# Kernel tuning notes

Measured on AMD Instinct MI355X. Metric: run time of the kernel, lower is better.

The kernel has to match this reference:

```python
import jax, jax.numpy as jnp
import numpy as np
import math

B, S, D, H = 2, 2048, 1024, 16
HD = D // H
EPS = 1e-05


def gelu(x):
    # tanh-approx GELU as in the torch source
    return 0.5 * x * (1.0 + jnp.tanh(jnp.sqrt(2.0 / jnp.pi) * (x + 0.044715 * x ** 3)))


def layernorm(x, w, b):
    # NOTE: torch .std() uses Bessel correction (ddof=1) and eps is added to std
    u = jnp.mean(x, axis=-1, keepdims=True)
    xc = x - u
    s = jnp.sqrt(jnp.sum(xc * xc, axis=-1, keepdims=True) / (x.shape[-1] - 1))
    return w * (xc / (s + EPS)) + b


def setup_inputs() -> dict:
    key = jax.random.key(0)
    ks = jax.random.split(key, 8)
    std = 0.02
    # weights stored [in, out] (transposed vs torch Linear) so y = x @ W + b
    return {
        "x": jax.random.normal(ks[0], (B, S, D), jnp.float32),
        "ln1_w": jnp.ones((D,), jnp.float32),
        "ln1_b": jnp.zeros((D,), jnp.float32),
        "c_attn_w": jax.random.normal(ks[1], (D, 3 * D), jnp.float32) * std,
        "c_attn_b": jnp.zeros((3 * D,), jnp.float32),
        "c_proj_w": jax.random.normal(ks[2], (D, D), jnp.float32) * std,
        "c_proj_b": jnp.zeros((D,), jnp.float32),
        "ln2_w": jnp.ones((D,), jnp.float32),
        "ln2_b": jnp.zeros((D,), jnp.float32),
        "fc_w": jax.random.normal(ks[3], (D, 4 * D), jnp.float32) * std,
        "fc_b": jnp.zeros((4 * D,), jnp.float32),
        "proj_w": jax.random.normal(ks[4], (4 * D, D), jnp.float32) * std,
        "proj_b": jnp.zeros((D,), jnp.float32),
    }


def attention(x, c_attn_w, c_attn_b, c_proj_w, c_proj_b):
    qkv = x @ c_attn_w + c_attn_b                      # [B,S,3D]
    q, k, v = jnp.split(qkv, 3, axis=-1)
    q = q.reshape(B, S, H, HD)
    k = k.reshape(B, S, H, HD)
    v = v.reshape(B, S, H, HD)
    w = jnp.einsum("bqhd,bkhd->bhqk", q, k) / math.sqrt(HD)  # scale=True
    bias = jnp.tril(jnp.ones((S, S), jnp.float32))     # causal mask
    w = w * bias - 1e10 * (1.0 - bias)
    w = jax.nn.softmax(w, axis=-1)
    a = jnp.einsum("bhqk,bkhd->bqhd", w, v).reshape(B, S, D)
    return a @ c_proj_w + c_proj_b


def reference(x, ln1_w, ln1_b, c_attn_w, c_attn_b, c_proj_w, c_proj_b,
              ln2_w, ln2_b, fc_w, fc_b, proj_w, proj_b):
    a = attention(layernorm(x, ln1_w, ln1_b), c_attn_w, c_attn_b, c_proj_w, c_proj_b)
    x = x + a
    h = gelu(layernorm(x, ln2_w, ln2_b) @ fc_w + fc_b)
    m = h @ proj_w + proj_b
    return x + m
```

## Files before the change

### kernel.cpp

```cpp
#include <hip/hip_runtime.h>

typedef unsigned short u16;
typedef __attribute__((ext_vector_type(8))) short short8;
typedef __attribute__((ext_vector_type(4))) float floatx4;

__device__ __forceinline__ float bf2f(u16 u) {
  unsigned int v = ((unsigned int)u) << 16;
  return __builtin_bit_cast(float, v);
}
__device__ __forceinline__ u16 f2bf(float f) {
  unsigned int u = __builtin_bit_cast(unsigned int, f);
  u += 0x7FFFu + ((u >> 16) & 1u);
  return (u16)(u >> 16);
}
__device__ __forceinline__ void gload_lds16(const void* g, void* l) {
  __builtin_amdgcn_global_load_lds(
      (const __attribute__((address_space(1))) unsigned int*)g,
      (__attribute__((address_space(3))) unsigned int*)l, 16, 0, 0);
}

__global__ __launch_bounds__(256) void transpose_f32_bf16(const float* __restrict__ in,
                                                          u16* __restrict__ out,
                                                          int K, int N) {
  __shared__ float tile[32][33];
  int n0 = blockIdx.x * 32, k0 = blockIdx.y * 32;
  int tx = threadIdx.x & 31, ty = threadIdx.x >> 5;
#pragma unroll
  for (int i = 0; i < 4; i++) {
    int r = ty + i * 8;
    tile[r][tx] = in[(size_t)(k0 + r) * N + n0 + tx];
  }
  __syncthreads();
#pragma unroll
  for (int i = 0; i < 4; i++) {
    int r = ty + i * 8;
    out[(size_t)(n0 + r) * K + k0 + tx] = f2bf(tile[tx][r]);
  }
}

__global__ __launch_bounds__(256) void ln_f32(const float* __restrict__ xin,
                                              const float* __restrict__ wgt,
                                              const float* __restrict__ bia,
                                              u16* __restrict__ out) {
  int row = blockIdx.x, t = threadIdx.x;
  const float* xr = xin + (size_t)row * 1024 + t * 4;
  float4 f = *(const float4*)xr;
  float v[4] = {f.x, f.y, f.z, f.w};
  float s1 = v[0] + v[1] + v[2] + v[3];
  float s2 = v[0] * v[0] + v[1] * v[1] + v[2] * v[2] + v[3] * v[3];
#pragma unroll
  for (int off = 32; off; off >>= 1) {
    s1 += __shfl_down(s1, off);
    s2 += __shfl_down(s2, off);
  }
  __shared__ float red[8];
  int lane = t & 63, w = t >> 6;
  if (lane == 0) { red[w] = s1; red[4 + w] = s2; }
  __syncthreads();
  s1 = red[0] + red[1] + red[2] + red[3];
  s2 = red[4] + red[5] + red[6] + red[7];
  float mean = s1 * (1.f / 1024.f);
  float var = (s2 - 1024.f * mean * mean) * (1.f / 1023.f);
  var = var < 0.f ? 0.f : var;
  float inv = 1.f / (sqrtf(var) + 1e-5f);
  float4 wv = *(const float4*)(wgt + t * 4);
  float4 bv = *(const float4*)(bia + t * 4);
  float wa[4] = {wv.x, wv.y, wv.z, wv.w};
  float ba[4] = {bv.x, bv.y, bv.z, bv.w};
#pragma unroll
  for (int j = 0; j < 4; j++)
    out[(size_t)row * 1024 + t * 4 + j] = f2bf(wa[j] * ((v[j] - mean) * inv) + ba[j]);
}

template <int EPI>
__global__ __launch_bounds__(256) void gemm_bt(const u16* __restrict__ A,
                                               const u16* __restrict__ Bt,
                                               const float* __restrict__ bias,
                                               const float* __restrict__ res,
                                               void* __restrict__ outp,
                                               void* __restrict__ outp2,
                                               int msplit,
                                               int ldc, int K) {
  __shared__ __align__(16) u16 As[2][128 * 64];
  __shared__ __align__(16) u16 Bs[2][128 * 64];
  int tid = threadIdx.x;
  int lane = tid & 63, w = tid >> 6;
  int quad = lane >> 4, c16 = lane & 15;
  int wm = w >> 1, wn = w & 1;
  int nbx = gridDim.x;
  int nwg = nbx * gridDim.y;
  int bid = blockIdx.y * nbx + blockIdx.x;
  int swz = (bid & 7) * (nwg >> 3) + (bid >> 3);
  int bn = swz % nbx, bm = swz / nbx;
  const u16* Ab = A + (size_t)bm * 128 * K;
  const u16* Bb = Bt + (size_t)bn * 128 * K;

  int rbase = tid >> 3;
  int csrc = (((tid & 7) ^ ((tid >> 3) & 7))) * 8;
  int dbase = w * 512;

  floatx4 zf = {0.f, 0.f, 0.f, 0.f};
  floatx4 acc[4][4];
#pragma unroll
  for (int i = 0; i < 4; i++)
#pragma unroll
    for (int j = 0; j < 4; j++) acc[i][j] = zf;

  auto stage = [&](int kt, int sl) {
    const u16* At = Ab + kt * 64;
    const u16* Bt2 = Bb + kt * 64;
#pragma unroll
    for (int j = 0; j < 4; j++) {
      int r = j * 32 + rbase;
      gload_lds16(At + (size_t)r * K + csrc, &As[sl][j * 2048 + dbase]);
      gload_lds16(Bt2 + (size_t)r * K + csrc, &Bs[sl][j * 2048 + dbase]);
    }
  };

  int nt = K >> 6;
  stage(0, 0);
  int sl = 0;
  for (int t = 0; t < nt; ++t) {
    if (t + 1 < nt) {
      stage(t + 1, sl ^ 1);
      asm volatile("s_waitcnt vmcnt(8)" ::: "memory");
    } else {
      asm volatile("s_waitcnt vmcnt(0)" ::: "memory");
    }
    __builtin_amdgcn_s_barrier();
    __builtin_amdgcn_sched_barrier(0);
    const u16* as = As[sl];
    const u16* bs = Bs[sl];
#pragma unroll
    for (int ks = 0; ks < 2; ++ks) {
      int col = (ks * 32 + quad * 8) ^ ((c16 & 7) * 8);
      short8 af[4], bfr[4];
#pragma unroll
      for (int mt = 0; mt < 4; mt++)
        af[mt] = *(const short8*)&as[(wm * 64 + mt * 16 + c16) * 64 + col];
#pragma unroll
      for (int nt2 = 0; nt2 < 4; nt2++)
        bfr[nt2] = *(const short8*)&bs[(wn * 64 + nt2 * 16 + c16) * 64 + col];
#pragma unroll
      for (int mt = 0; mt < 4; mt++)
#pragma unroll
        for (int nt2 = 0; nt2 < 4; nt2++)
          acc[mt][nt2] = __builtin_amdgcn_mfma_f32_16x16x32_bf16(af[mt], bfr[nt2], acc[mt][nt2], 0, 0, 0);
    }
    __builtin_amdgcn_s_barrier();
    __builtin_amdgcn_sched_barrier(0);
    sl ^= 1;
  }

  int gm0 = bm * 128 + wm * 64;
  int gn0 = bn * 128 + wn * 64;
#pragma unroll
  for (int nt2 = 0; nt2 < 4; nt2++) {
    int gn = gn0 + nt2 * 16 + c16;
    float bia = 0.f;
    if constexpr (EPI != 3) bia = bias[gn];
#pragma unroll
    for (int mt = 0; mt < 4; mt++) {
#pragma unroll
      for (int r = 0; r < 4; r++) {
        int gm = gm0 + mt * 16 + quad * 4 + r;
        float v = acc[mt][nt2][r] + bia;
        if constexpr (EPI == 0) {
          void* op = outp;
          int gmo = gm;
          if (gm >= msplit) { op = outp2; gmo = gm - msplit; }
          ((u16*)op)[(size_t)gmo * ldc + gn] = f2bf(v);
        } else if constexpr (EPI == 1) {
          size_t o = (size_t)gm * ldc + gn;
          ((float*)outp)[o] = v + res[o];
        } else if constexpr (EPI == 2) {
          size_t o = (size_t)gm * ldc + gn;
          float g = 0.5f * v * (1.f + tanhf(0.7978845608f * (v + 0.044715f * v * v * v)));
          ((u16*)outp)[o] = f2bf(g);
        } else {
          size_t o = (size_t)gm * ldc + gn;
          ((float*)outp)[o] += v;
        }
      }
    }
  }
}

__device__ __forceinline__ void attn_process(
    const short8& qf0, const short8& qf1,
    float* m_run, float* l_run, floatx4* oacc,
    const u16* __restrict__ Ks, const u16* __restrict__ Vt, u16* __restrict__ pw,
    int kt, int qt, int w, int quad, int c16, bool diag) {
  floatx4 zf = {0.f, 0.f, 0.f, 0.f};
  floatx4 s[4];
#pragma unroll
  for (int n = 0; n < 4; n++) {
    short8 kf0 = *(const short8*)&Ks[(n * 16 + c16) * 72 + quad * 8];
    short8 kf1 = *(const short8*)&Ks[(n * 16 + c16) * 72 + 32 + quad * 8];
    floatx4 a = zf;
    a = __builtin_amdgcn_mfma_f32_16x16x32_bf16(qf0, kf0, a, 0, 0, 0);
    a = __builtin_amdgcn_mfma_f32_16x16x32_bf16(qf1, kf1, a, 0, 0, 0);
    s[n] = a;
  }
  if (diag) {
#pragma unroll
    for (int n = 0; n < 4; n++) {
      int kg = kt * 64 + n * 16 + c16;
#pragma unroll
      for (int r = 0; r < 4; r++) {
        int qg = qt * 64 + w * 16 + quad * 4 + r;
        s[n][r] = (kg > qg) ? -1e30f : s[n][r];
      }
    }
  }
  float mt[4];
#pragma unroll
  for (int r = 0; r < 4; r++)
    mt[r] = fmaxf(fmaxf(s[0][r], s[1][r]), fmaxf(s[2][r], s[3][r]));
#pragma unroll
  for (int off = 1; off < 16; off <<= 1)
#pragma unroll
    for (int r = 0; r < 4; r++) mt[r] = fmaxf(mt[r], __shfl_xor(mt[r], off));
  float alpha[4], lsum[4];
#pragma unroll
  for (int r = 0; r < 4; r++) {
    float mn = fmaxf(m_run[r], mt[r]);
    alpha[r] = __expf(m_run[r] - mn);
    m_run[r] = mn;
    lsum[r] = 0.f;
  }
#pragma unroll
  for (int n = 0; n < 4; n++)
#pragma unroll
    for (int r = 0; r < 4; r++) {
      float p = __expf(s[n][r] - m_run[r]);
      s[n][r] = p;
      lsum[r] += p;
    }
#pragma unroll
  for (int off = 1; off < 16; off <<= 1)
#pragma unroll
    for (int r = 0; r < 4; r++) lsum[r] += __shfl_xor(lsum[r], off);
#pragma unroll
  for (int r = 0; r < 4; r++) l_run[r] = l_run[r] * alpha[r] + lsum[r];
#pragma unroll
  for (int c = 0; c < 4; c++)
#pragma unroll
    for (int r = 0; r < 4; r++) oacc[c][r] *= alpha[r];
#pragma unroll
  for (int n = 0; n < 4; n++)
#pragma unroll
    for (int r = 0; r < 4; r++)
      pw[(quad * 4 + r) * 72 + n * 16 + c16] = f2bf(s[n][r]);
  short8 pf0 = *(const short8*)&pw[c16 * 72 + quad * 8];
  short8 pf1 = *(const short8*)&pw[c16 * 72 + 32 + quad * 8];
#pragma unroll
  for (int c = 0; c < 4; c++) {
    int d = c * 16 + c16;
    short8 vf0 = *(const short8*)&Vt[d * 64 + ((quad * 8) ^ (d & 56))];
    short8 vf1 = *(const short8*)&Vt[d * 64 + ((32 + quad * 8) ^ (d & 56))];
    oacc[c] = __builtin_amdgcn_mfma_f32_16x16x32_bf16(pf0, vf0, oacc[c], 0, 0, 0);
    oacc[c] = __builtin_amdgcn_mfma_f32_16x16x32_bf16(pf1, vf1, oacc[c], 0, 0, 0);
  }
}

__device__ __forceinline__ short8 scale8_eighth(short8 v) {
  short8 r;
#pragma unroll
  for (int j = 0; j < 8; j++) {
    unsigned int b = ((unsigned int)(u16)v[j]) << 16;
    float f = __builtin_bit_cast(float, b) * 0.125f;
    r[j] = (short)(u16)(__builtin_bit_cast(unsigned int, f) >> 16);
  }
  return r;
}

__global__ __launch_bounds__(256) void attn_mfma2(const u16* __restrict__ qkv0,
                                                  const u16* __restrict__ qkv1,
                                                  u16* __restrict__ aout) {
  int pr = blockIdx.x, h = blockIdx.y;
  const u16* qkvb = blockIdx.z ? qkv1 : qkv0;
  aout += (size_t)blockIdx.z * 2048 * 1024;
  int qt0 = pr, qt1 = 31 - pr;
  int tid = threadIdx.x, lane = tid & 63, w = tid >> 6;
  int quad = lane >> 4, c16 = lane & 15;
  __shared__ __align__(16) u16 Ks[2][64 * 72];
  __shared__ __align__(16) u16 Vt[2][64 * 64];
  __shared__ __align__(16) u16 Ps[4][16 * 72];

  size_t qoffA = (size_t)(qt0 * 64 + w * 16 + c16) * 3072 + h * 64;
  short8 qfA0 = scale8_eighth(*(const short8*)(qkvb + qoffA + quad * 8));
  short8 qfA1 = scale8_eighth(*(const short8*)(qkvb + qoffA + 32 + quad * 8));
  size_t qoffB = (size_t)(qt1 * 64 + w * 16 + c16) * 3072 + h * 64;
  short8 qfB0 = scale8_eighth(*(const short8*)(qkvb + qoffB + quad * 8));
  short8 qfB1 = scale8_eighth(*(const short8*)(qkvb + qoffB + 32 + quad * 8));

  floatx4 zf = {0.f, 0.f, 0.f, 0.f};
  float mA[4], lA[4], mB[4], lB[4];
  floatx4 oA[4], oB[4];
#pragma unroll
  for (int r = 0; r < 4; r++) { mA[r] = -1e30f; lA[r] = 0.f; mB[r] = -1e30f; lB[r] = 0.f; }
#pragma unroll
  for (int c = 0; c < 4; c++) { oA[c] = zf; oB[c] = zf; }

  int srow = (tid * 2) >> 3;
  int sd8 = ((tid * 2) & 7) * 8;
  short8 kr0, kr1, vr0, vr1;

  auto issue = [&](int kt) {
    size_t gb = (size_t)(kt * 64 + srow) * 3072 + h * 64 + sd8;
    kr0 = *(const short8*)(qkvb + gb + 1024);
    kr1 = *(const short8*)(qkvb + gb + 1024 + 8);
    vr0 = *(const short8*)(qkvb + gb + 2048);
    vr1 = *(const short8*)(qkvb + gb + 2048 + 8);
  };
  auto commit = [&](int b) {
    *(short8*)&Ks[b][srow * 72 + sd8] = kr0;
    *(short8*)&Ks[b][srow * 72 + sd8 + 8] = kr1;
    u16* vt = Vt[b];
#pragma unroll
    for (int j = 0; j < 8; j++) {
      int d = sd8 + j;
      vt[d * 64 + (srow ^ (d & 56))] = (u16)vr0[j];
      int d2 = sd8 + 8 + j;
      vt[d2 * 64 + (srow ^ (d2 & 56))] = (u16)vr1[j];
    }
  };

  u16* pw = &Ps[w][0];
  int last = qt1;
  issue(0);
  commit(0);
  __syncthreads();
  int cur = 0;
  for (int kt = 0; kt <= last; ++kt) {
    if (kt < last) issue(kt + 1);

    attn_process(qfB0, qfB1, mB, lB, oB, Ks[cur], Vt[cur], pw, kt, qt1, w, quad, c16, kt == qt1);
    if (kt <= qt0)
      attn_process(qfA0, qfA1, mA, lA, oA, Ks[cur], Vt[cur], pw, kt, qt0, w, quad, c16, kt == qt0);

    if (kt < last) {
      commit(cur ^ 1);
      __syncthreads();
      cur ^= 1;
    }
  }

  size_t obA = (size_t)(qt0 * 64 + w * 16) * 1024 + h * 64;
  size_t obB = (size_t)(qt1 * 64 + w * 16) * 1024 + h * 64;
#pragma unroll
  for (int r = 0; r < 4; r++) {
    float invA = 1.f / lA[r], invB = 1.f / lB[r];
#pragma unroll
    for (int c = 0; c < 4; c++) {
      aout[obA + (size_t)(quad * 4 + r) * 1024 + c * 16 + c16] = f2bf(oA[c][r] * invA);
      aout[obB + (size_t)(quad * 4 + r) * 1024 + c * 16 + c16] = f2bf(oB[c][r] * invB);
    }
  }
}

extern "C" void kernel_launch(void* const* d_in, const int* in_sizes, int n_in,
                              void* d_out, int out_size, void* d_ws, size_t ws_size,
                              hipStream_t stream) {
  const float* x        = (const float*)d_in[0];
  const float* ln1_w    = (const float*)d_in[1];
  const float* ln1_b    = (const float*)d_in[2];
  const float* c_attn_w = (const float*)d_in[3];
  const float* c_attn_b = (const float*)d_in[4];
  const float* c_proj_w = (const float*)d_in[5];
  const float* c_proj_b = (const float*)d_in[6];
  const float* ln2_w    = (const float*)d_in[7];
  const float* ln2_b    = (const float*)d_in[8];
  const float* fc_w     = (const float*)d_in[9];
  const float* fc_b     = (const float*)d_in[10];
  const float* proj_w   = (const float*)d_in[11];
  const float* proj_b   = (const float*)d_in[12];

  char* ws = (char*)d_ws;
  const size_t MiB = 1u << 20;
  const int BIG = 1 << 30;

  u16* wt_attn  = (u16*)(ws + 0);
  u16* wt_cproj = (u16*)(ws + 6 * MiB);
  u16* ln1b     = (u16*)(ws + 8 * MiB);
  u16* qkv1     = (u16*)(ws + 16 * MiB);
  u16* qkv0     = (u16*)d_out;
  u16* attn_out = (u16*)(ws + 8 * MiB);
  float* x1     = (float*)d_out;

  transpose_f32_bf16<<<dim3(96, 32), 256, 0, stream>>>(c_attn_w, wt_attn, 1024, 3072);
  transpose_f32_bf16<<<dim3(32, 32), 256, 0, stream>>>(c_proj_w, wt_cproj, 1024, 1024);
  ln_f32<<<4096, 256, 0, stream>>>(x, ln1_w, ln1_b, ln1b);
  gemm_bt<0><<<dim3(24, 32), 256, 0, stream>>>(ln1b, wt_attn, c_attn_b, nullptr,
                                               qkv0, qkv1, 2048, 3072, 1024);
  attn_mfma2<<<dim3(16, 16, 2), 256, 0, stream>>>(qkv0, qkv1, attn_out);
  gemm_bt<1><<<dim3(8, 32), 256, 0, stream>>>(attn_out, wt_cproj, c_proj_b, x,
                                              x1, nullptr, BIG, 1024, 1024);

  int NC = (ws_size >= 58720256) ? 1 : (ws_size >= 37748736) ? 2 : 4;
  int CN = 4096 / NC;
  u16* wt_fc = (u16*)(ws + 0);
  u16* ln2b  = (u16*)(ws + 8 * MiB);
  u16* h_c   = (u16*)(ws + 16 * MiB);
  u16* projT = (u16*)(ws + 16 * MiB + (size_t)4096 * CN * 2);

  transpose_f32_bf16<<<dim3(128, 32), 256, 0, stream>>>(fc_w, wt_fc, 1024, 4096);
  ln_f32<<<4096, 256, 0, stream>>>(x1, ln2_w, ln2_b, ln2b);
  for (int c = 0; c < NC; c++) {
    transpose_f32_bf16<<<dim3(32, CN / 32), 256, 0, stream>>>(
        proj_w + (size_t)c * CN * 1024, projT, CN, 1024);
    gemm_bt<2><<<dim3(CN / 128, 32), 256, 0, stream>>>(
        ln2b, wt_fc + (size_t)c * CN * 1024, fc_b + c * CN, nullptr,
        h_c, nullptr, BIG, CN, 1024);
    if (NC == 1)
      gemm_bt<1><<<dim3(8, 32), 256, 0, stream>>>(h_c, projT, proj_b, x1,
                                                  x1, nullptr, BIG, 1024, CN);
    else if (c < NC - 1)
      gemm_bt<3><<<dim3(8, 32), 256, 0, stream>>>(h_c, projT, nullptr, nullptr,
                                                  x1, nullptr, BIG, 1024, CN);
    else
      gemm_bt<4><<<dim3(8, 32), 256, 0, stream>>>(h_c, projT, proj_b, nullptr,
                                                  x1, nullptr, BIG, 1024, CN);
  }
}
```

Before: 399.5 us.

## Split paired query tiles across two warp groups in 512-thread attention blocks

The attention kernel now launches 512 threads per block. Warps 0-3 handle the far query tile (qt1) and warps 4-7 handle the near tile (qt0), where before each of 4 warps processed both tiles one after the other. K/V staging is spread over twice as many threads, and the P scratch buffer doubles to 8 slots. This raises per-block parallelism and cuts per-thread register state. The cost is that the qt0 warps sit idle after their tile's causal range ends while still joining every barrier.

New measurement: 392.8 us. Within noise of the previous version (-1.7%).

```diff
diff --git a/kernel.cpp b/kernel.cpp
--- a/kernel.cpp
+++ b/kernel.cpp
@@ -190,7 +190,7 @@
     const short8& qf0, const short8& qf1,
     float* m_run, float* l_run, floatx4* oacc,
     const u16* __restrict__ Ks, const u16* __restrict__ Vt, u16* __restrict__ pw,
-    int kt, int qt, int w, int quad, int c16, bool diag) {
+    int kt, int qt, int wrow, int quad, int c16, bool diag) {
   floatx4 zf = {0.f, 0.f, 0.f, 0.f};
   floatx4 s[4];
 #pragma unroll
@@ -208,7 +208,7 @@
       int kg = kt * 64 + n * 16 + c16;
 #pragma unroll
       for (int r = 0; r < 4; r++) {
-        int qg = qt * 64 + w * 16 + quad * 4 + r;
+        int qg = qt * 64 + wrow * 16 + quad * 4 + r;
         s[n][r] = (kg > qg) ? -1e30f : s[n][r];
       }
     }
@@ -275,7 +275,7 @@
   return r;
 }
 
-__global__ __launch_bounds__(256) void attn_mfma2(const u16* __restrict__ qkv0,
+__global__ __launch_bounds__(512) void attn_mfma2(const u16* __restrict__ qkv0,
                                                   const u16* __restrict__ qkv1,
                                                   u16* __restrict__ aout) {
   int pr = blockIdx.x, h = blockIdx.y;
@@ -284,79 +284,69 @@
   int qt0 = pr, qt1 = 31 - pr;
   int tid = threadIdx.x, lane = tid & 63, w = tid >> 6;
   int quad = lane >> 4, c16 = lane & 15;
+  int wrow = w & 3, tb = w >> 2;
+  int qt_my = tb ? qt0 : qt1;
   __shared__ __align__(16) u16 Ks[2][64 * 72];
   __shared__ __align__(16) u16 Vt[2][64 * 64];
-  __shared__ __align__(16) u16 Ps[4][16 * 72];
-
-  size_t qoffA = (size_t)(qt0 * 64 + w * 16 + c16) * 3072 + h * 64;
-  short8 qfA0 = scale8_eighth(*(const short8*)(qkvb + qoffA + quad * 8));
-  short8 qfA1 = scale8_eighth(*(const short8*)(qkvb + qoffA + 32 + quad * 8));
-  size_t qoffB = (size_t)(qt1 * 64 + w * 16 + c16) * 3072 + h * 64;
-  short8 qfB0 = scale8_eighth(*(const short8*)(qkvb + qoffB + quad * 8));
-  short8 qfB1 = scale8_eighth(*(const short8*)(qkvb + qoffB + 32 + quad * 8));
+  __shared__ __align__(16) u16 Ps[8][16 * 72];
+
+  size_t qoff = (size_t)(qt_my * 64 + wrow * 16 + c16) * 3072 + h * 64;
+  short8 qf0 = scale8_eighth(*(const short8*)(qkvb + qoff + quad * 8));
+  short8 qf1 = scale8_eighth(*(const short8*)(qkvb + qoff + 32 + quad * 8));
 
   floatx4 zf = {0.f, 0.f, 0.f, 0.f};
-  float mA[4], lA[4], mB[4], lB[4];
-  floatx4 oA[4], oB[4];
-#pragma unroll
-  for (int r = 0; r < 4; r++) { mA[r] = -1e30f; lA[r] = 0.f; mB[r] = -1e30f; lB[r] = 0.f; }
-#pragma unroll
-  for (int c = 0; c < 4; c++) { oA[c] = zf; oB[c] = zf; }
-
-  int srow = (tid * 2) >> 3;
-  int sd8 = ((tid * 2) & 7) * 8;
-  short8 kr0, kr1, vr0, vr1;
+  float m[4], l[4];
+  floatx4 o[4];
+#pragma unroll
+  for (int r = 0; r < 4; r++) { m[r] = -1e30f; l[r] = 0.f; }
+#pragma unroll
+  for (int c = 0; c < 4; c++) o[c] = zf;
+
+  int srow = tid >> 3;
+  int sd8 = (tid & 7) * 8;
+  short8 kr, vr;
 
   auto issue = [&](int kt) {
     size_t gb = (size_t)(kt * 64 + srow) * 3072 + h * 64 + sd8;
-    kr0 = *(const short8*)(qkvb + gb + 1024);
-    kr1 = *(const short8*)(qkvb + gb + 1024 + 8);
-    vr0 = *(const short8*)(qkvb + gb + 2048);
-    vr1 = *(const short8*)(qkvb + gb + 2048 + 8);
+    kr = *(const short8*)(qkvb + gb + 1024);
+    vr = *(const short8*)(qkvb + gb + 2048);
   };
   auto commit = [&](int b) {
-    *(short8*)&Ks[b][srow * 72 + sd8] = kr0;
-    *(short8*)&Ks[b][srow * 72 + sd8 + 8] = kr1;
+    *(short8*)&Ks[b][srow * 72 + sd8] = kr;
     u16* vt = Vt[b];
 #pragma unroll
     for (int j = 0; j < 8; j++) {
       int d = sd8 + j;
-      vt[d * 64 + (srow ^ (d & 56))] = (u16)vr0[j];
-      int d2 = sd8 + 8 + j;
-      vt[d2 * 64 + (srow ^ (d2 & 56))] = (u16)vr1[j];
+      vt[d * 64 + (srow ^ (d & 56))] = (u16)vr[j];
     }
   };
 
   u16* pw = &Ps[w][0];
-  int last = qt1;
   issue(0);
   commit(0);
   __syncthreads();
   int cur = 0;
-  for (int kt = 0; kt <= last; ++kt) {
-    if (kt < last) issue(kt + 1);
-
-    attn_process(qfB0, qfB1, mB, lB, oB, Ks[cur], Vt[cur], pw, kt, qt1, w, quad, c16, kt == qt1);
-    if (kt <= qt0)
-      attn_process(qfA0, qfA1, mA, lA, oA, Ks[cur], Vt[cur], pw, kt, qt0, w, quad, c16, kt == qt0);
-
-    if (kt < last) {
+  for (int kt = 0; kt <= qt1; ++kt) {
+    if (kt < qt1) issue(kt + 1);
+
+    if (tb == 0 || kt <= qt0)
+      attn_process(qf0, qf1, m, l, o, Ks[cur], Vt[cur], pw, kt, qt_my, wrow,
+                   quad, c16, kt == qt_my);
+
+    if (kt < qt1) {
       commit(cur ^ 1);
       __syncthreads();
       cur ^= 1;
     }
   }
 
-  size_t obA = (size_t)(qt0 * 64 + w * 16) * 1024 + h * 64;
-  size_t obB = (size_t)(qt1 * 64 + w * 16) * 1024 + h * 64;
+  size_t ob = (size_t)(qt_my * 64 + wrow * 16) * 1024 + h * 64;
 #pragma unroll
   for (int r = 0; r < 4; r++) {
-    float invA = 1.f / lA[r], invB = 1.f / lB[r];
-#pragma unroll
-    for (int c = 0; c < 4; c++) {
-      aout[obA + (size_t)(quad * 4 + r) * 1024 + c * 16 + c16] = f2bf(oA[c][r] * invA);
-      aout[obB + (size_t)(quad * 4 + r) * 1024 + c * 16 + c16] = f2bf(oB[c][r] * invB);
-    }
+    float inv = 1.f / l[r];
+#pragma unroll
+    for (int c = 0; c < 4; c++)
+      aout[ob + (size_t)(quad * 4 + r) * 1024 + c * 16 + c16] = f2bf(o[c][r] * inv);
   }
 }
 
@@ -394,7 +384,7 @@
   ln_f32<<<4096, 256, 0, stream>>>(x, ln1_w, ln1_b, ln1b);
   gemm_bt<0><<<dim3(24, 32), 256, 0, stream>>>(ln1b, wt_attn, c_attn_b, nullptr,
                                                qkv0, qkv1, 2048, 3072, 1024);
-  attn_mfma2<<<dim3(16, 16, 2), 256, 0, stream>>>(qkv0, qkv1, attn_out);
+  attn_mfma2<<<dim3(16, 16, 2), 512, 0, stream>>>(qkv0, qkv1, attn_out);
   gemm_bt<1><<<dim3(8, 32), 256, 0, stream>>>(attn_out, wt_cproj, c_proj_b, x,
                                               x1, nullptr, BIG, 1024, 1024);
 
```
